# Optimization experiments

Measured on AMD Instinct MI355X. Metric: run time of the kernel, lower is better.

## Reference

```python
import jax, jax.numpy as jnp
import numpy as np

Z, K, HID = 128, 256, 512  # z_size, key_size, hidden_size


def setup_inputs() -> dict:
    key = jax.random.key(0)
    ks = jax.random.split(key, 12)
    B, T, Hi, Wi, Y = 512, 32, 32, 32, 4
    D = Hi * Wi
    s = 0.02
    f32 = jnp.float32
    return {
        "x_seq": jax.random.normal(ks[0], (B, T, Hi, Wi), f32),
        "W_enc": jax.random.normal(ks[1], (D, Z), f32) * s,
        "b_enc": jnp.zeros((Z,), f32),
        "W_lstm": jax.random.normal(ks[2], (K + 1, 4 * HID), f32) * s,
        "U_lstm": jax.random.normal(ks[3], (HID, 4 * HID), f32) * s,
        "b_lstm": jnp.zeros((4 * HID,), f32),
        "W_key": jax.random.normal(ks[4], (HID, K), f32) * s,
        "b_key": jnp.zeros((K,), f32),
        "W_g": jax.random.normal(ks[5], (HID, 1), f32) * s,
        "b_g": jnp.zeros((1,), f32),
        "W_y": jax.random.normal(ks[6], (HID, Y), f32) * s,
        "b_y": jnp.zeros((Y,), f32),
        "gamma": jnp.ones((Z,), f32),
        "beta": jnp.zeros((Z,), f32),
        "conf_gain": jnp.float32(1.0),
        "conf_bias": jnp.float32(0.0),
    }


def _forward(x_seq, W_enc, b_enc, W_lstm, U_lstm, b_lstm, W_key, b_key,
             W_g, b_g, W_y, b_y, gamma, beta, conf_gain, conf_bias):
    B, T = x_seq.shape[0], x_seq.shape[1]
    N = T + 1  # memory slots after final null step
    x = x_seq.reshape(B, T, -1)
    z = jax.nn.relu(x @ W_enc + b_enc)  # (B,T,Z) encoder stand-in
    # Faithful to TF source: list of (B,Z) stacks to (T,B,Z) and reduce axis 1
    # -> normalization is over the BATCH axis.
    mu = jnp.mean(z, axis=0, keepdims=True)
    var = jnp.var(z, axis=0, keepdims=True)
    z = (z - mu) / jnp.sqrt(var + 1e-8) * gamma + beta
    z_full = jnp.concatenate([z, jnp.zeros((B, 1, Z), z.dtype)], axis=1)  # (B,N,Z)

    def lstm_cell(x_in, h_in, c_in):
        gates = x_in @ W_lstm + h_in @ U_lstm + b_lstm
        i, f, g_, o = jnp.split(gates, 4, axis=-1)  # keras gate order i,f,c,o
        c_new = jax.nn.sigmoid(f) * c_in + jax.nn.sigmoid(i) * jnp.tanh(g_)
        h_new = jax.nn.sigmoid(o) * jnp.tanh(c_new)
        return h_new, c_new

    slot_ids = jnp.arange(N)

    def step(carry, inp):
        h, c, key_r, M_k, M_v = carry
        z_t, t = inp  # z_t: (B,Z), t: scalar step index
        # Faithful: source passes initial_state=(cell_state, hidden), swapping roles.
        h_new, c_new = lstm_cell(key_r, c, h)
        key_w = jax.nn.relu(h_new @ W_key + b_key)          # (B,K)
        g = jax.nn.sigmoid(h_new @ W_g + b_g)               # (B,1)
        y_lin = jax.nn.softmax(h_new @ W_y + b_y, axis=-1)  # (B,Y)
        # content-addressable read over the t filled slots
        sim = jnp.einsum('bz,bnz->bn', z_t, M_v)            # (B,N)
        mask = (slot_ids < t)[None, :]
        w_k = jax.nn.softmax(jnp.where(mask, sim, -1e9), axis=1)
        c_k = jax.nn.sigmoid(sim * conf_gain + conf_bias)   # (B,N)
        mem = jnp.concatenate([M_k, c_k[..., None]], axis=2)  # (B,N,K+1)
        weighted = jnp.einsum('bn,bnp->bp', w_k, mem)       # (B,K+1)
        key_r_new = jnp.where(t == 0, jnp.zeros_like(key_r), g * weighted)
        # write into slot t (pre-allocated memory, masked read above)
        M_k = M_k.at[:, t, :].set(key_w)
        M_v = M_v.at[:, t, :].set(z_t)
        return (h_new, c_new, key_r_new, M_k, M_v), y_lin

    h0 = jnp.zeros((B, HID), z.dtype)
    c0 = jnp.zeros((B, HID), z.dtype)
    kr0 = jnp.zeros((B, K + 1), z.dtype)
    Mk0 = jnp.zeros((B, N, K), z.dtype)
    Mv0 = jnp.zeros((B, N, Z), z.dtype)
    xs = (jnp.swapaxes(z_full, 0, 1), slot_ids)
    _, ys = jax.lax.scan(step, (h0, c0, kr0, Mk0, Mv0), xs)
    return ys[-1]  # y_pred_linear from the final (null-input) step


def reference(x_seq, W_enc, b_enc, W_lstm, U_lstm, b_lstm, W_key, b_key,
              W_g, b_g, W_y, b_y, gamma, beta, conf_gain, conf_bias):
    return _forward(x_seq, W_enc, b_enc, W_lstm, U_lstm, b_lstm, W_key, b_key,
                    W_g, b_g, W_y, b_y, gamma, beta, conf_gain, conf_bias)
```

## Files before the change

kernel.cpp:

```cpp
#include <hip/hip_runtime.h>

typedef __attribute__((ext_vector_type(8))) short short8;
typedef __attribute__((ext_vector_type(4))) float f32x4;
typedef __attribute__((ext_vector_type(8))) unsigned short ushort8;
typedef __attribute__((ext_vector_type(4))) unsigned short ushort4v;

__device__ __forceinline__ unsigned short f2bf(float f) {
  union { float f; unsigned u; } v; v.f = f;
  unsigned u = v.u;
  u += 0x7fffu + ((u >> 16) & 1u);
  return (unsigned short)(u >> 16);
}
__device__ __forceinline__ float sigm(float x) { return 1.f / (1.f + __expf(-x)); }
__device__ __forceinline__ float ftanh(float x) { return 1.f - 2.f / (__expf(2.f * x) + 1.f); }

__device__ __forceinline__ void gl16(const unsigned short* g, unsigned short* l) {
  __builtin_amdgcn_global_load_lds((const __attribute__((address_space(1))) void*)g,
                                   (__attribute__((address_space(3))) void*)l, 16, 0, 0);
}

__device__ __forceinline__ uint4 ld16_sys(const void* base, int off) {
  uint4 r;
  asm volatile("global_load_dwordx4 %0, %1, %2 sc0 sc1"
               : "=v"(r) : "v"(off), "s"(base) : "memory");
  return r;
}
__device__ __forceinline__ uint4 ld16_asm(const void* base, int off) {
  uint4 r;
  asm volatile("global_load_dwordx4 %0, %1, %2"
               : "=v"(r) : "v"(off), "s"(base) : "memory");
  return r;
}
__device__ __forceinline__ float ldf_sys(const void* base, int off) {
  float r;
  asm volatile("global_load_dword %0, %1, %2 sc0 sc1"
               : "=v"(r) : "v"(off), "s"(base) : "memory");
  return r;
}
__device__ __forceinline__ unsigned ldu_sys(const void* base, int off) {
  unsigned r;
  asm volatile("global_load_dword %0, %1, %2 sc0 sc1"
               : "=v"(r) : "v"(off), "s"(base) : "memory");
  return r;
}
__device__ __forceinline__ void stf_sys(void* base, int off, float v) {
  asm volatile("global_store_dword %0, %1, %2 sc0 sc1"
               :: "v"(off), "v"(v), "s"(base) : "memory");
}
__device__ __forceinline__ void stu_sys(void* base, int off, unsigned v) {
  asm volatile("global_store_dword %0, %1, %2 sc0 sc1"
               :: "v"(off), "v"(v), "s"(base) : "memory");
}
__device__ __forceinline__ void sth_sys(void* base, int off, unsigned short v) {
  asm volatile("global_store_short %0, %1, %2 sc0 sc1"
               :: "v"(off), "v"(v), "s"(base) : "memory");
}
#define WAITVM(N)                                          \
  asm volatile("s_waitcnt vmcnt(" #N ")" ::: "memory");    \
  __builtin_amdgcn_sched_barrier(0)

__device__ __forceinline__ void gbar(unsigned* flags, unsigned gen) {
  asm volatile("s_waitcnt vmcnt(0)" ::: "memory");
  __syncthreads();
  if (threadIdx.x == 0) stu_sys(flags, (int)(blockIdx.x * 64), gen);
  int off = (int)(threadIdx.x * 64);
  for (;;) {
    unsigned v = ldu_sys(flags, off);
    asm volatile("s_waitcnt vmcnt(0)" ::: "memory");
    if (v >= gen) break;
    __builtin_amdgcn_s_sleep(1);
  }
  __syncthreads();
}

#define LSTR 40

__global__ void k_prep(const float* __restrict__ W_lstm, const float* __restrict__ U_lstm,
                       const float* __restrict__ W_enc, const float* __restrict__ W_key,
                       const float* __restrict__ W_g, const float* __restrict__ W_y,
                       const float* __restrict__ b_key, const float* __restrict__ b_g,
                       const float* __restrict__ b_y,
                       unsigned short* __restrict__ WcombT, unsigned short* __restrict__ Wk2T,
                       unsigned short* __restrict__ WencT, float* __restrict__ bias2,
                       unsigned short* __restrict__ xinA, unsigned short* __restrict__ xinB,
                       float* __restrict__ h, float* __restrict__ z_full,
                       unsigned* __restrict__ bar) {
  const int N1 = 2048 * 800, N2 = 320 * 512, N3 = 128 * 1024, N4 = 320,
            N5 = 512 * 800, N7 = 512 * 512, N8 = 512 * 128, N9 = 4096;
  int i = blockIdx.x * 256 + threadIdx.x;
  if (i < N1) {
    int np = i / 800, k = i - np * 800;
    int j = np >> 2, gate = np & 3, n = gate * 512 + j;
    float v = 0.f;
    if (k < 257) v = W_lstm[k * 2048 + n];
    else if (k >= 288) v = U_lstm[(k - 288) * 2048 + n];
    WcombT[i] = f2bf(v);
    return;
  }
  i -= N1;
  if (i < N2) {
    int n = i / 512, k = i - n * 512;
    float v = 0.f;
    if (n < 256) v = W_key[k * 256 + n];
    else if (n == 256) v = W_g[k];
    else if (n < 261) v = W_y[k * 4 + (n - 257)];
    Wk2T[i] = f2bf(v);
    return;
  }
  i -= N2;
  if (i < N3) {
    int n = i / 1024, k = i - n * 1024;
    WencT[i] = f2bf(W_enc[k * 128 + n]);
    return;
  }
  i -= N3;
  if (i < N4) {
    float v = (i < 256) ? b_key[i] : (i == 256 ? b_g[0] : (i < 261 ? b_y[i - 257] : 0.f));
    bias2[i] = v;
    return;
  }
  i -= N4;
  if (i < N5) { xinA[i] = 0; return; }
  i -= N5;
  if (i < N5) { xinB[i] = 0; return; }
  i -= N5;
  if (i < N7) { h[i] = 0.f; return; }
  i -= N7;
  if (i < N8) {
    int b = i >> 7, z = i & 127;
    z_full[(b * 33 + 32) * 128 + z] = 0.f;
    return;
  }
  i -= N8;
  if (i < N9) bar[i] = 0;
}

__global__ __launch_bounds__(512) void k_enc(const float* __restrict__ x,
                                             const unsigned short* __restrict__ WencT,
                                             const float* __restrict__ b_enc,
                                             float* __restrict__ zbuf) {
  __shared__ __align__(16) unsigned short As[2][64 * LSTR];
  __shared__ __align__(16) unsigned short Bs[2][128 * LSTR];
  int tid = threadIdx.x;
  int m0 = blockIdx.x * 64;
  int lane = tid & 63, wid = tid >> 6;
  int wm = (wid >> 2) * 32, wn = (wid & 3) * 32;
  int q = lane >> 4, r = lane & 15;
  int ldrowA = tid >> 3, ldcA = (tid & 7) * 4;
  int ldrowB = tid >> 2, ldcB = (tid & 3) * 8;
  const float4* Ag = reinterpret_cast<const float4*>(x + (size_t)(m0 + ldrowA) * 1024);
  const uint4* Bg = reinterpret_cast<const uint4*>(WencT + (size_t)ldrowB * 1024);
  float4 ra = Ag[ldcA >> 2];
  uint4 rb = Bg[ldcB >> 3];
  f32x4 acc[2][2] = {};
  int s = 0;
  {
    ushort4v t4;
    t4[0] = f2bf(ra.x); t4[1] = f2bf(ra.y); t4[2] = f2bf(ra.z); t4[3] = f2bf(ra.w);
    *reinterpret_cast<ushort4v*>(&As[0][ldrowA * LSTR + ldcA]) = t4;
    *reinterpret_cast<uint4*>(&Bs[0][ldrowB * LSTR + ldcB]) = rb;
  }
  __syncthreads();
  for (int kk = 0; kk < 32; ++kk) {
    if (kk < 31) {
      int k0 = (kk + 1) * 32;
      ra = Ag[(k0 + ldcA) >> 2];
      rb = Bg[(k0 + ldcB) >> 3];
    }
    short8 a0 = *reinterpret_cast<const short8*>(&As[s][(wm + r) * LSTR + q * 8]);
    short8 a1 = *reinterpret_cast<const short8*>(&As[s][(wm + 16 + r) * LSTR + q * 8]);
    short8 b0 = *reinterpret_cast<const short8*>(&Bs[s][(wn + r) * LSTR + q * 8]);
    short8 b1 = *reinterpret_cast<const short8*>(&Bs[s][(wn + 16 + r) * LSTR + q * 8]);
    acc[0][0] = __builtin_amdgcn_mfma_f32_16x16x32_bf16(a0, b0, acc[0][0], 0, 0, 0);
    acc[0][1] = __builtin_amdgcn_mfma_f32_16x16x32_bf16(a0, b1, acc[0][1], 0, 0, 0);
    acc[1][0] = __builtin_amdgcn_mfma_f32_16x16x32_bf16(a1, b0, acc[1][0], 0, 0, 0);
    acc[1][1] = __builtin_amdgcn_mfma_f32_16x16x32_bf16(a1, b1, acc[1][1], 0, 0, 0);
    if (kk < 31) {
      ushort4v t4;
      t4[0] = f2bf(ra.x); t4[1] = f2bf(ra.y); t4[2] = f2bf(ra.z); t4[3] = f2bf(ra.w);
      *reinterpret_cast<ushort4v*>(&As[s ^ 1][ldrowA * LSTR + ldcA]) = t4;
      *reinterpret_cast<uint4*>(&Bs[s ^ 1][ldrowB * LSTR + ldcB]) = rb;
      s ^= 1;
    }
    __syncthreads();
  }
#pragma unroll
  for (int mt = 0; mt < 2; ++mt)
#pragma unroll
    for (int nt = 0; nt < 2; ++nt)
#pragma unroll
      for (int e = 0; e < 4; ++e) {
        int row = m0 + wm + mt * 16 + q * 4 + e;
        int col = wn + nt * 16 + r;
        zbuf[(size_t)row * 128 + col] = fmaxf(acc[mt][nt][e] + b_enc[col], 0.f);
      }
}

__global__ __launch_bounds__(256) void k_ln(const float* __restrict__ zbuf,
                                            const float* __restrict__ gamma,
                                            const float* __restrict__ beta,
                                            float* __restrict__ z_full) {
  int bid = blockIdx.x;
  int tstep = bid >> 3;
  int z0 = (bid & 7) * 16;
  int tid = threadIdx.x;
  int zl = tid & 15, bg = tid >> 4;
  __shared__ float ps[256], qs[256];
  __shared__ float muS[16], rsS[16];
  float s = 0.f, ss = 0.f;
  for (int ii = 0; ii < 32; ++ii) {
    int b = bg * 32 + ii;
    float v = zbuf[(size_t)(b * 32 + tstep) * 128 + z0 + zl];
    s += v; ss += v * v;
  }
  ps[tid] = s; qs[tid] = ss;
  __syncthreads();
  if (tid < 16) {
    float S = 0.f, Q = 0.f;
    for (int g2 = 0; g2 < 16; ++g2) { S += ps[g2 * 16 + tid]; Q += qs[g2 * 16 + tid]; }
    float mu = S / 512.f;
    float var = Q / 512.f - mu * mu;
    muS[tid] = mu;
    rsS[tid] = rsqrtf(var + 1e-8f);
  }
  __syncthreads();
  float ga = gamma[z0 + zl], be = beta[z0 + zl];
  float mu = muS[zl], rs = rsS[zl];
  for (int ii = 0; ii < 32; ++ii) {
    int b = bg * 32 + ii;
    float v = zbuf[(size_t)(b * 32 + tstep) * 128 + z0 + zl];
    z_full[(size_t)(b * 33 + tstep) * 128 + z0 + zl] = (v - mu) * rs * ga + be;
  }
}

__global__ __launch_bounds__(256) void k_attnpre(const float* __restrict__ z_full,
                                                 const float* __restrict__ cgain,
                                                 const float* __restrict__ cbias,
                                                 float* __restrict__ wk_tbl,
                                                 float* __restrict__ wck_tbl) {
  __shared__ float zs[33 * 128];
  __shared__ float sim[33 * 33];
  int b = blockIdx.x, tid = threadIdx.x;
  const float* zb = z_full + (size_t)b * 33 * 128;
  for (int i = tid; i < 33 * 128; i += 256) zs[i] = zb[i];
  __syncthreads();
  for (int p = tid; p < 33 * 33; p += 256) {
    int t = p / 33, n = p - t * 33;
    float s = 0.f;
    if (n < t) {
#pragma unroll 8
      for (int k2 = 0; k2 < 128; ++k2) s += zs[t * 128 + k2] * zs[n * 128 + k2];
    }
    sim[p] = s;
  }
  __syncthreads();
  if (tid >= 1 && tid < 33) {
    int t = tid;
    float cg = cgain[0], cb2 = cbias[0];
    float m = -3.0e38f;
    for (int n = 0; n < t; ++n) m = fmaxf(m, sim[t * 33 + n]);
    float ssum = 0.f;
    for (int n = 0; n < t; ++n) ssum += __expf(sim[t * 33 + n] - m);
    float inv = 1.f / ssum;
    float wck = 0.f;
    for (int n = 0; n < t; ++n) {
      float wk = __expf(sim[t * 33 + n] - m) * inv;
      wk_tbl[((size_t)b * 33 + t) * 33 + n] = wk;
      float ck = 1.f / (1.f + __expf(-(sim[t * 33 + n] * cg + cb2)));
      wck += wk * ck;
    }
    wck_tbl[b * 33 + t] = wck;
  }
}

__global__ __launch_bounds__(256) void k_loop(
    unsigned short* __restrict__ xinA, unsigned short* __restrict__ xinB,
    const unsigned short* __restrict__ WT, const float* __restrict__ b_lstm,
    float* __restrict__ h, unsigned short* __restrict__ hbf,
    const unsigned short* __restrict__ Wk2T, const float* __restrict__ bias2,
    float* __restrict__ Mk, float* __restrict__ logits,
    const float* __restrict__ Wg, const float* __restrict__ bg,
    const float* __restrict__ wk_tbl, const float* __restrict__ wck_tbl,
    float* __restrict__ out, unsigned* __restrict__ bar) {
  __shared__ __align__(16) unsigned short Bres[64 * 808];
  __shared__ __align__(16) unsigned char scr[43136];
  const int tid = threadIdx.x, bid = blockIdx.x;
  const int lane = tid & 63, w = tid >> 6;
  const int q = lane >> 4, r = lane & 15;
  const int wm = (w >> 1) * 32, wn = (w & 1) * 32;
  const int nn = bid & 31, mi = bid >> 5;
  const int m0 = mi * 64, n0g = nn * 64;
  unsigned gen = 0;

  for (int l = 0; l < 26; ++l) {
    int gw = l * 256 + w * 64;
    if (gw < 6464) {
      int g = gw + lane;
      int row = g / 101, cg = g - row * 101;
      int col = (cg >= 100) ? 792 : cg * 8;
      gl16(WT + (size_t)(n0g + row) * 800 + col, Bres + gw * 8);
    }
  }

  int srow[5], scol[5];
#pragma unroll
  for (int l = 0; l < 5; ++l) {
    int idx = l * 256 + tid;
    srow[l] = idx / 20;
    scol[l] = (idx - srow[l] * 20) * 8;
  }
  unsigned short* A0 = (unsigned short*)scr;
  unsigned short* A1 = (unsigned short*)(scr + 21504);

  const int jl = tid & 15, jg = nn * 16 + jl, rl0 = tid >> 4;
  const float bL0 = b_lstm[jg], bL1 = b_lstm[512 + jg],
              bL2 = b_lstm[1024 + jg], bL3 = b_lstm[1536 + jg];
  float hreg[4] = {0.f, 0.f, 0.f, 0.f};

  const int mi2 = bid / 5, ni2 = bid - mi2 * 5;

  asm volatile("s_waitcnt vmcnt(0)" ::: "memory");
  __syncthreads();

  for (int t = 0; t < 33; ++t) {
    const unsigned short* cur = (t & 1) ? xinB : xinA;
    unsigned short* nxt = (t & 1) ? xinA : xinB;

    uint4 R[5];
#pragma unroll
    for (int l = 0; l < 5; ++l)
      R[l] = ld16_sys(cur, ((m0 + srow[l]) * 800 + scol[l]) * 2);
    asm volatile("s_waitcnt vmcnt(0)" ::: "memory");
    __builtin_amdgcn_sched_barrier(0);
#pragma unroll
    for (int l = 0; l < 5; ++l)
      *(uint4*)&A0[srow[l] * 168 + scol[l]] = R[l];
    __syncthreads();

    f32x4 acc[2][2] = {};
    for (int c = 0; c < 5; ++c) {
      const unsigned short* Ac = (c & 1) ? A1 : A0;
      unsigned short* An = (c & 1) ? A0 : A1;
      if (c < 4) {
#pragma unroll
        for (int l = 0; l < 5; ++l)
          R[l] = ld16_sys(cur, ((m0 + srow[l]) * 800 + (c + 1) * 160 + scol[l]) * 2);
      }
#pragma unroll
      for (int ks = 0; ks < 5; ++ks) {
        short8 a0 = *(const short8*)&Ac[(wm + r) * 168 + ks * 32 + q * 8];
        short8 a1 = *(const short8*)&Ac[(wm + 16 + r) * 168 + ks * 32 + q * 8];
        short8 b0 = *(const short8*)&Bres[(wn + r) * 808 + c * 160 + ks * 32 + q * 8];
        short8 b1 = *(const short8*)&Bres[(wn + 16 + r) * 808 + c * 160 + ks * 32 + q * 8];
        acc[0][0] = __builtin_amdgcn_mfma_f32_16x16x32_bf16(a0, b0, acc[0][0], 0, 0, 0);
        acc[0][1] = __builtin_amdgcn_mfma_f32_16x16x32_bf16(a0, b1, acc[0][1], 0, 0, 0);
        acc[1][0] = __builtin_amdgcn_mfma_f32_16x16x32_bf16(a1, b0, acc[1][0], 0, 0, 0);
        acc[1][1] = __builtin_amdgcn_mfma_f32_16x16x32_bf16(a1, b1, acc[1][1], 0, 0, 0);
      }
      if (c < 4) {
        asm volatile("s_waitcnt vmcnt(0)" ::: "memory");
        __builtin_amdgcn_sched_barrier(0);
#pragma unroll
        for (int l = 0; l < 5; ++l)
          *(uint4*)&An[srow[l] * 168 + scol[l]] = R[l];
        __syncthreads();
      }
    }
    __syncthreads();

    float* Cs = (float*)scr;
#pragma unroll
    for (int mt = 0; mt < 2; ++mt)
#pragma unroll
      for (int nt = 0; nt < 2; ++nt)
#pragma unroll
        for (int e = 0; e < 4; ++e)
          Cs[(wm + mt * 16 + q * 4 + e) * 65 + wn + nt * 16 + r] = acc[mt][nt][e];
    __syncthreads();
#pragma unroll
    for (int it = 0; it < 4; ++it) {
      int rl = it * 16 + rl0;
      int brow = m0 + rl;
      float gi = Cs[rl * 65 + jl * 4 + 0] + bL0;
      float gf = Cs[rl * 65 + jl * 4 + 1] + bL1;
      float gc = Cs[rl * 65 + jl * 4 + 2] + bL2;
      float go = Cs[rl * 65 + jl * 4 + 3] + bL3;
      float cnew = sigm(gf) * hreg[it] + sigm(gi) * ftanh(gc);
      float hnew = sigm(go) * ftanh(cnew);
      hreg[it] = hnew;
      stf_sys(h, (brow * 512 + jg) * 4, hnew);
      sth_sys(hbf, (brow * 512 + jg) * 2, f2bf(hnew));
      sth_sys(nxt, (brow * 800 + 288 + jg) * 2, f2bf(cnew));
    }
    ++gen; gbar(bar, gen);

    if (bid < 40) {
      int m0b = mi2 * 64, n0b = ni2 * 64;
      int aoff0 = ((m0b + wm + r) * 512 + q * 8) * 2;
      int aoff1 = aoff0 + 16 * 1024;
      int boff0 = ((n0b + wn + r) * 512 + q * 8) * 2;
      int boff1 = boff0 + 16 * 1024;
      uint4 ab[4][2], bb[4][2];
      f32x4 acc2[2][2] = {};
#pragma unroll
      for (int j = 0; j < 3; ++j) {
        ab[j][0] = ld16_sys(hbf, aoff0 + j * 64);
        ab[j][1] = ld16_sys(hbf, aoff1 + j * 64);
        bb[j][0] = ld16_asm(Wk2T, boff0 + j * 64);
        bb[j][1] = ld16_asm(Wk2T, boff1 + j * 64);
      }
#pragma unroll
      for (int kk = 0; kk < 16; ++kk) {
        if (kk < 13) {
          int j = kk + 3;
          ab[j & 3][0] = ld16_sys(hbf, aoff0 + j * 64);
          ab[j & 3][1] = ld16_sys(hbf, aoff1 + j * 64);
          bb[j & 3][0] = ld16_asm(Wk2T, boff0 + j * 64);
          bb[j & 3][1] = ld16_asm(Wk2T, boff1 + j * 64);
        }
        if (kk < 13) { WAITVM(12); }
        else if (kk == 13) { WAITVM(8); }
        else if (kk == 14) { WAITVM(4); }
        else { WAITVM(0); }
        short8 a0 = *(const short8*)&ab[kk & 3][0];
        short8 a1 = *(const short8*)&ab[kk & 3][1];
        short8 b0s = *(const short8*)&bb[kk & 3][0];
        short8 b1s = *(const short8*)&bb[kk & 3][1];
        acc2[0][0] = __builtin_amdgcn_mfma_f32_16x16x32_bf16(a0, b0s, acc2[0][0], 0, 0, 0);
        acc2[0][1] = __builtin_amdgcn_mfma_f32_16x16x32_bf16(a0, b1s, acc2[0][1], 0, 0, 0);
        acc2[1][0] = __builtin_amdgcn_mfma_f32_16x16x32_bf16(a1, b0s, acc2[1][0], 0, 0, 0);
        acc2[1][1] = __builtin_amdgcn_mfma_f32_16x16x32_bf16(a1, b1s, acc2[1][1], 0, 0, 0);
      }
#pragma unroll
      for (int mt = 0; mt < 2; ++mt)
#pragma unroll
        for (int nt = 0; nt < 2; ++nt)
#pragma unroll
          for (int e2 = 0; e2 < 4; ++e2) {
            int row = m0b + wm + mt * 16 + q * 4 + e2;
            int np = n0b + wn + nt * 16 + r;
            float v = acc2[mt][nt][e2] + bias2[np];
            if (np < 256)
              stf_sys(Mk, ((row * 33 + t) * 256 + np) * 4, fmaxf(v, 0.f));
            else if (np >= 257 && np < 261)
              stf_sys(logits, (row * 4 + (np - 257)) * 4, v);
          }
    } else if (t > 0 && t < 32) {
      float* wkS = (float*)scr;
      float* red4 = (float*)(scr + 512);
      for (int rr = 0; rr < 3; ++rr) {
        int b = (bid - 40) + 216 * rr;
        if (b < 512) {
          float ha = ldf_sys(h, (b * 512 + tid) * 4);
          float hb = ldf_sys(h, (b * 512 + 256 + tid) * 4);
          asm volatile("s_waitcnt vmcnt(0)" ::: "memory");
          float sd = ha * Wg[tid] + hb * Wg[256 + tid];
#pragma unroll
          for (int off = 32; off > 0; off >>= 1) sd += __shfl_down(sd, off);
          if (lane == 0) red4[w] = sd;
          if (tid < t) wkS[tid] = wk_tbl[((size_t)b * 33 + t) * 33 + tid];
          __syncthreads();
          float g = 1.f / (1.f + __expf(-(red4[0] + red4[1] + red4[2] + red4[3] + bg[0])));
          float p0 = 0.f, p1 = 0.f, p2 = 0.f, p3 = 0.f;
          int n = 0;
          for (; n + 4 <= t; n += 4) {
            p0 += wkS[n] * Mk[((size_t)b * 33 + n) * 256 + tid];
            p1 += wkS[n + 1] * Mk[((size_t)b * 33 + n + 1) * 256 + tid];
            p2 += wkS[n + 2] * Mk[((size_t)b * 33 + n + 2) * 256 + tid];
            p3 += wkS[n + 3] * Mk[((size_t)b * 33 + n + 3) * 256 + tid];
          }
          for (; n < t; ++n) p0 += wkS[n] * Mk[((size_t)b * 33 + n) * 256 + tid];
          sth_sys(nxt, (b * 800 + tid) * 2, f2bf(g * ((p0 + p1) + (p2 + p3))));
          if (tid == 0) sth_sys(nxt, (b * 800 + 256) * 2, f2bf(g * wck_tbl[b * 33 + t]));
          __syncthreads();
        }
      }
    }
    ++gen; gbar(bar, gen);
  }
  if (bid == 0) {
    for (int r2 = tid; r2 < 512; r2 += 256) {
      float a = ldf_sys(logits, r2 * 16);
      float b2 = ldf_sys(logits, r2 * 16 + 4);
      float c2 = ldf_sys(logits, r2 * 16 + 8);
      float d2 = ldf_sys(logits, r2 * 16 + 12);
      asm volatile("s_waitcnt vmcnt(0)" ::: "memory");
      float m = fmaxf(fmaxf(a, b2), fmaxf(c2, d2));
      float ea = __expf(a - m), eb = __expf(b2 - m), ec = __expf(c2 - m), ed = __expf(d2 - m);
      float ssum = ea + eb + ec + ed;
      out[r2 * 4] = ea / ssum; out[r2 * 4 + 1] = eb / ssum;
      out[r2 * 4 + 2] = ec / ssum; out[r2 * 4 + 3] = ed / ssum;
    }
  }
}

__global__ __launch_bounds__(256) void k_gates(const unsigned short* __restrict__ xin,
                                               const unsigned short* __restrict__ WT,
                                               const float* __restrict__ b_lstm,
                                               float* __restrict__ h,
                                               unsigned short* __restrict__ hbf,
                                               unsigned short* __restrict__ xin_nxt) {
  __shared__ __align__(16) unsigned short As[2][64 * LSTR];
  __shared__ __align__(16) unsigned short Bs[2][64 * LSTR];
  __shared__ float Cs[64 * 65];
  int tid = threadIdx.x;
  int nn = blockIdx.x;
  int m0 = blockIdx.y * 64;
  int n0 = nn * 64;
  int lane = tid & 63, wid = tid >> 6;
  int wm = (wid >> 1) * 32, wn = (wid & 1) * 32;
  int q = lane >> 4, r = lane & 15;
  int ldrow = tid >> 2, ldc = (tid & 3) * 8;
  const uint4* Ag = reinterpret_cast<const uint4*>(xin + (size_t)(m0 + ldrow) * 800);
  const uint4* Bg = reinterpret_cast<const uint4*>(WT + (size_t)(n0 + ldrow) * 800);
  uint4 ra = Ag[ldc >> 3], rb = Bg[ldc >> 3];
  f32x4 acc[2][2] = {};
  int s = 0;
  *reinterpret_cast<uint4*>(&As[0][ldrow * LSTR + ldc]) = ra;
  *reinterpret_cast<uint4*>(&Bs[0][ldrow * LSTR + ldc]) = rb;
  __syncthreads();
  for (int kk = 0; kk < 25; ++kk) {
    if (kk < 24) {
      int k0 = (kk + 1) * 32;
      ra = Ag[(k0 + ldc) >> 3];
      rb = Bg[(k0 + ldc) >> 3];
    }
    short8 a0 = *reinterpret_cast<const short8*>(&As[s][(wm + r) * LSTR + q * 8]);
    short8 a1 = *reinterpret_cast<const short8*>(&As[s][(wm + 16 + r) * LSTR + q * 8]);
    short8 b0 = *reinterpret_cast<const short8*>(&Bs[s][(wn + r) * LSTR + q * 8]);
    short8 b1 = *reinterpret_cast<const short8*>(&Bs[s][(wn + 16 + r) * LSTR + q * 8]);
    acc[0][0] = __builtin_amdgcn_mfma_f32_16x16x32_bf16(a0, b0, acc[0][0], 0, 0, 0);
    acc[0][1] = __builtin_amdgcn_mfma_f32_16x16x32_bf16(a0, b1, acc[0][1], 0, 0, 0);
    acc[1][0] = __builtin_amdgcn_mfma_f32_16x16x32_bf16(a1, b0, acc[1][0], 0, 0, 0);
    acc[1][1] = __builtin_amdgcn_mfma_f32_16x16x32_bf16(a1, b1, acc[1][1], 0, 0, 0);
    if (kk < 24) {
      *reinterpret_cast<uint4*>(&As[s ^ 1][ldrow * LSTR + ldc]) = ra;
      *reinterpret_cast<uint4*>(&Bs[s ^ 1][ldrow * LSTR + ldc]) = rb;
      s ^= 1;
    }
    __syncthreads();
  }
#pragma unroll
  for (int mt = 0; mt < 2; ++mt)
#pragma unroll
    for (int nt = 0; nt < 2; ++nt)
#pragma unroll
      for (int e = 0; e < 4; ++e)
        Cs[(wm + mt * 16 + q * 4 + e) * 65 + wn + nt * 16 + r] = acc[mt][nt][e];
  __syncthreads();
#pragma unroll
  for (int it = 0; it < 4; ++it) {
    int id = it * 256 + tid;
    int rl = id >> 4, jl = id & 15;
    int brow = m0 + rl;
    int j = nn * 16 + jl;
    float gi = Cs[rl * 65 + jl * 4 + 0] + b_lstm[j];
    float gf = Cs[rl * 65 + jl * 4 + 1] + b_lstm[512 + j];
    float gg = Cs[rl * 65 + jl * 4 + 2] + b_lstm[1024 + j];
    float go = Cs[rl * 65 + jl * 4 + 3] + b_lstm[1536 + j];
    float hold = h[brow * 512 + j];
    float cnew = sigm(gf) * hold + sigm(gi) * ftanh(gg);
    float hnew = sigm(go) * ftanh(cnew);
    h[brow * 512 + j] = hnew;
    hbf[brow * 512 + j] = f2bf(hnew);
    xin_nxt[brow * 800 + 288 + j] = f2bf(cnew);
  }
}

__global__ __launch_bounds__(256) void k_head(const unsigned short* __restrict__ hbf,
                                              const unsigned short* __restrict__ Wk2T,
                                              const float* __restrict__ bias2,
                                              float* __restrict__ Mk,
                                              float* __restrict__ logits,
                                              const float* __restrict__ h,
                                              const float* __restrict__ Wg,
                                              const float* __restrict__ bg,
                                              const float* __restrict__ wk_tbl,
                                              const float* __restrict__ wck_tbl,
                                              unsigned short* __restrict__ xin_nxt,
                                              int t) {
  __shared__ __align__(16) unsigned short As[2][64 * LSTR];
  __shared__ __align__(16) unsigned short Bs[2][64 * LSTR];
  __shared__ float wkS[33];
  __shared__ float red[256];
  int bid = blockIdx.x;
  int tid = threadIdx.x;
  if (bid < 40) {
    int mi = bid / 5, ni = bid - mi * 5;
    int m0 = mi * 64, n0 = ni * 64;
    int lane = tid & 63, wid = tid >> 6;
    int wm = (wid >> 1) * 32, wn = (wid & 1) * 32;
    int q = lane >> 4, r = lane & 15;
    int ldrow = tid >> 2, ldc = (tid & 3) * 8;
    const uint4* Ag = reinterpret_cast<const uint4*>(hbf + (size_t)(m0 + ldrow) * 512);
    const uint4* Bg = reinterpret_cast<const uint4*>(Wk2T + (size_t)(n0 + ldrow) * 512);
    uint4 ra = Ag[ldc >> 3], rb = Bg[ldc >> 3];
    f32x4 acc[2][2] = {};
    int s = 0;
    *reinterpret_cast<uint4*>(&As[0][ldrow * LSTR + ldc]) = ra;
    *reinterpret_cast<uint4*>(&Bs[0][ldrow * LSTR + ldc]) = rb;
    __syncthreads();
    for (int kk = 0; kk < 16; ++kk) {
      if (kk < 15) {
        int k0 = (kk + 1) * 32;
        ra = Ag[(k0 + ldc) >> 3];
        rb = Bg[(k0 + ldc) >> 3];
      }
      short8 a0 = *reinterpret_cast<const short8*>(&As[s][(wm + r) * LSTR + q * 8]);
      short8 a1 = *reinterpret_cast<const short8*>(&As[s][(wm + 16 + r) * LSTR + q * 8]);
      short8 b0 = *reinterpret_cast<const short8*>(&Bs[s][(wn + r) * LSTR + q * 8]);
      short8 b1 = *reinterpret_cast<const short8*>(&Bs[s][(wn + 16 + r) * LSTR + q * 8]);
      acc[0][0] = __builtin_amdgcn_mfma_f32_16x16x32_bf16(a0, b0, acc[0][0], 0, 0, 0);
      acc[0][1] = __builtin_amdgcn_mfma_f32_16x16x32_bf16(a0, b1, acc[0][1], 0, 0, 0);
      acc[1][0] = __builtin_amdgcn_mfma_f32_16x16x32_bf16(a1, b0, acc[1][0], 0, 0, 0);
      acc[1][1] = __builtin_amdgcn_mfma_f32_16x16x32_bf16(a1, b1, acc[1][1], 0, 0, 0);
      if (kk < 15) {
        *reinterpret_cast<uint4*>(&As[s ^ 1][ldrow * LSTR + ldc]) = ra;
        *reinterpret_cast<uint4*>(&Bs[s ^ 1][ldrow * LSTR + ldc]) = rb;
        s ^= 1;
      }
      __syncthreads();
    }
#pragma unroll
    for (int mt = 0; mt < 2; ++mt)
#pragma unroll
      for (int nt = 0; nt < 2; ++nt)
#pragma unroll
        for (int e = 0; e < 4; ++e) {
          int row = m0 + wm + mt * 16 + q * 4 + e;
          int np = n0 + wn + nt * 16 + r;
          float v = acc[mt][nt][e] + bias2[np];
          if (np < 256) Mk[(size_t)(row * 33 + t) * 256 + np] = fmaxf(v, 0.f);
          else if (np >= 257 && np < 261) logits[row * 4 + (np - 257)] = v;
        }
  } else {
    if (t == 0 || t == 32) return;
    int b = bid - 40;
    float s = h[b * 512 + tid] * Wg[tid] + h[b * 512 + 256 + tid] * Wg[256 + tid];
    red[tid] = s;
    if (tid < t) wkS[tid] = wk_tbl[((size_t)b * 33 + t) * 33 + tid];
    __syncthreads();
    for (int off = 128; off > 0; off >>= 1) {
      if (tid < off) red[tid] += red[tid + off];
      __syncthreads();
    }
    float g = 1.f / (1.f + __expf(-(red[0] + bg[0])));
    float acc = 0.f;
    for (int n = 0; n < t; ++n) acc += wkS[n] * Mk[((size_t)b * 33 + n) * 256 + tid];
    xin_nxt[b * 800 + tid] = f2bf(g * acc);
    if (tid == 0) xin_nxt[b * 800 + 256] = f2bf(g * wck_tbl[b * 33 + t]);
  }
}

__global__ void k_softmax(const float* __restrict__ logits, float* __restrict__ out) {
  int tid = threadIdx.x;
  for (int r2 = tid; r2 < 512; r2 += 256) {
    float a = logits[r2 * 4], b = logits[r2 * 4 + 1], c = logits[r2 * 4 + 2], d = logits[r2 * 4 + 3];
    float m = fmaxf(fmaxf(a, b), fmaxf(c, d));
    float ea = __expf(a - m), eb = __expf(b - m), ec = __expf(c - m), ed = __expf(d - m);
    float s = ea + eb + ec + ed;
    out[r2 * 4] = ea / s; out[r2 * 4 + 1] = eb / s;
    out[r2 * 4 + 2] = ec / s; out[r2 * 4 + 3] = ed / s;
  }
}

extern "C" void kernel_launch(void* const* d_in, const int* in_sizes, int n_in,
                              void* d_out, int out_size, void* d_ws, size_t ws_size,
                              hipStream_t stream) {
  const float* x_seq = (const float*)d_in[0];
  const float* W_enc = (const float*)d_in[1];
  const float* b_enc = (const float*)d_in[2];
  const float* W_lstm = (const float*)d_in[3];
  const float* U_lstm = (const float*)d_in[4];
  const float* b_lstm = (const float*)d_in[5];
  const float* W_key = (const float*)d_in[6];
  const float* b_key = (const float*)d_in[7];
  const float* W_g = (const float*)d_in[8];
  const float* b_g = (const float*)d_in[9];
  const float* W_y = (const float*)d_in[10];
  const float* b_y = (const float*)d_in[11];
  const float* gamma = (const float*)d_in[12];
  const float* beta = (const float*)d_in[13];
  const float* cg_ = (const float*)d_in[14];
  const float* cb = (const float*)d_in[15];

  char* p = (char*)d_ws;
  auto alloc = [&](size_t bytes) {
    char* r = p;
    p += (bytes + 255) & ~(size_t)255;
    return r;
  };
  float* zbuf = (float*)alloc((size_t)16384 * 128 * 4);
  float* z_full = (float*)alloc((size_t)512 * 33 * 128 * 4);
  unsigned short* WcombT = (unsigned short*)alloc((size_t)2048 * 800 * 2);
  unsigned short* WencT = (unsigned short*)alloc((size_t)128 * 1024 * 2);
  unsigned short* Wk2T = (unsigned short*)alloc((size_t)320 * 512 * 2);
  float* bias2 = (float*)alloc(320 * 4);
  unsigned short* xinA = (unsigned short*)alloc((size_t)512 * 800 * 2);
  unsigned short* xinB = (unsigned short*)alloc((size_t)512 * 800 * 2);
  float* h = (float*)alloc((size_t)512 * 512 * 4);
  unsigned short* hbf = (unsigned short*)alloc((size_t)512 * 512 * 2);
  float* Mk = (float*)alloc((size_t)512 * 33 * 256 * 4);
  float* logits = (float*)alloc((size_t)512 * 4 * 4);
  float* wk_tbl = (float*)alloc((size_t)512 * 33 * 33 * 4);
  float* wck_tbl = (float*)alloc((size_t)512 * 33 * 4);
  unsigned* bar = (unsigned*)alloc(16384);
  float* outp = (float*)d_out;

  const int prep_total = 2048 * 800 + 320 * 512 + 128 * 1024 + 320 + 2 * 512 * 800 +
                         512 * 512 + 512 * 128 + 4096;
  k_prep<<<(prep_total + 255) / 256, 256, 0, stream>>>(
      W_lstm, U_lstm, W_enc, W_key, W_g, W_y, b_key, b_g, b_y,
      WcombT, Wk2T, WencT, bias2, xinA, xinB, h, z_full, bar);
  k_enc<<<256, 512, 0, stream>>>(x_seq, WencT, b_enc, zbuf);
  k_ln<<<256, 256, 0, stream>>>(zbuf, gamma, beta, z_full);
  k_attnpre<<<512, 256, 0, stream>>>(z_full, cg_, cb, wk_tbl, wck_tbl);

  void* cargs[16];
  cargs[0] = &xinA;  cargs[1] = &xinB;   cargs[2] = &WcombT; cargs[3] = &b_lstm;
  cargs[4] = &h;     cargs[5] = &hbf;    cargs[6] = &Wk2T;   cargs[7] = &bias2;
  cargs[8] = &Mk;    cargs[9] = &logits; cargs[10] = &W_g;   cargs[11] = &b_g;
  cargs[12] = &wk_tbl; cargs[13] = &wck_tbl; cargs[14] = &outp; cargs[15] = &bar;
  hipError_t ce = hipLaunchCooperativeKernel((const void*)k_loop, dim3(256), dim3(256),
                                             cargs, 0u, stream);
  if (ce != hipSuccess) {
    for (int t = 0; t < 33; ++t) {
      unsigned short* cur = (t & 1) ? xinB : xinA;
      unsigned short* nxt = (t & 1) ? xinA : xinB;
      k_gates<<<dim3(32, 8), 256, 0, stream>>>(cur, WcombT, b_lstm, h, hbf, nxt);
      k_head<<<552, 256, 0, stream>>>(hbf, Wk2T, bias2, Mk, logits, h,
                                      W_g, b_g, wk_tbl, wck_tbl, nxt, t);
    }
    k_softmax<<<1, 256, 0, stream>>>(logits, outp);
  }
}
```

Measured before the change: 782.7 us.

## Replace grid-wide barrier with per-batch-group barriers and fuse final softmax

Each group of 32 blocks owning the same 64 batch rows now does the gate GEMM, key projection and attention read for those rows, so the barrier only waits on the group's 32 flags instead of all 256 blocks. The key head now skips the logits column tile except on the final step, and that last step computes the softmax directly instead of a separate single-block pass after the loop. The trailing barrier on the last step is dropped. This cuts cross-CU synchronisation cost and per-step work, at the cost of a less even split of the attention work across blocks.

```diff
diff --git a/kernel.cpp b/kernel.cpp
--- a/kernel.cpp
+++ b/kernel.cpp
@@ -59,11 +59,12 @@
   asm volatile("s_waitcnt vmcnt(" #N ")" ::: "memory");    \
   __builtin_amdgcn_sched_barrier(0)
 
-__device__ __forceinline__ void gbar(unsigned* flags, unsigned gen) {
+__device__ __forceinline__ void gbar_grp(unsigned* flags, unsigned gen,
+                                         int myslot, int pollslot) {
   asm volatile("s_waitcnt vmcnt(0)" ::: "memory");
   __syncthreads();
-  if (threadIdx.x == 0) stu_sys(flags, (int)(blockIdx.x * 64), gen);
-  int off = (int)(threadIdx.x * 64);
+  if (threadIdx.x == 0) stu_sys(flags, myslot * 64, gen);
+  int off = pollslot * 64;
   for (;;) {
     unsigned v = ldu_sys(flags, off);
     asm volatile("s_waitcnt vmcnt(0)" ::: "memory");
@@ -278,25 +279,26 @@
     const unsigned short* __restrict__ WT, const float* __restrict__ b_lstm,
     float* __restrict__ h, unsigned short* __restrict__ hbf,
     const unsigned short* __restrict__ Wk2T, const float* __restrict__ bias2,
-    float* __restrict__ Mk, float* __restrict__ logits,
-    const float* __restrict__ Wg, const float* __restrict__ bg,
-    const float* __restrict__ wk_tbl, const float* __restrict__ wck_tbl,
-    float* __restrict__ out, unsigned* __restrict__ bar) {
+    float* __restrict__ Mk, const float* __restrict__ Wg,
+    const float* __restrict__ bg, const float* __restrict__ wk_tbl,
+    const float* __restrict__ wck_tbl, float* __restrict__ out,
+    unsigned* __restrict__ bar) {
   __shared__ __align__(16) unsigned short Bres[64 * 808];
   __shared__ __align__(16) unsigned char scr[43136];
   const int tid = threadIdx.x, bid = blockIdx.x;
   const int lane = tid & 63, w = tid >> 6;
   const int q = lane >> 4, r = lane & 15;
   const int wm = (w >> 1) * 32, wn = (w & 1) * 32;
-  const int nn = bid & 31, mi = bid >> 5;
-  const int m0 = mi * 64, n0g = nn * 64;
+  const int nn = bid & 31, g = bid >> 5;
+  const int m0 = g * 64, n0g = nn * 64;
+  const int pollslot = (g << 5) + (tid & 31);
   unsigned gen = 0;
 
   for (int l = 0; l < 26; ++l) {
     int gw = l * 256 + w * 64;
     if (gw < 6464) {
-      int g = gw + lane;
-      int row = g / 101, cg = g - row * 101;
+      int gg = gw + lane;
+      int row = gg / 101, cg = gg - row * 101;
       int col = (cg >= 100) ? 792 : cg * 8;
       gl16(WT + (size_t)(n0g + row) * 800 + col, Bres + gw * 8);
     }
@@ -316,8 +318,6 @@
   const float bL0 = b_lstm[jg], bL1 = b_lstm[512 + jg],
               bL2 = b_lstm[1024 + jg], bL3 = b_lstm[1536 + jg];
   float hreg[4] = {0.f, 0.f, 0.f, 0.f};
-
-  const int mi2 = bid / 5, ni2 = bid - mi2 * 5;
 
   asm volatile("s_waitcnt vmcnt(0)" ::: "memory");
   __syncthreads();
@@ -392,65 +392,94 @@
       sth_sys(hbf, (brow * 512 + jg) * 2, f2bf(hnew));
       sth_sys(nxt, (brow * 800 + 288 + jg) * 2, f2bf(cnew));
     }
-    ++gen; gbar(bar, gen);
-
-    if (bid < 40) {
-      int m0b = mi2 * 64, n0b = ni2 * 64;
-      int aoff0 = ((m0b + wm + r) * 512 + q * 8) * 2;
-      int aoff1 = aoff0 + 16 * 1024;
-      int boff0 = ((n0b + wn + r) * 512 + q * 8) * 2;
-      int boff1 = boff0 + 16 * 1024;
-      uint4 ab[4][2], bb[4][2];
-      f32x4 acc2[2][2] = {};
-#pragma unroll
-      for (int j = 0; j < 3; ++j) {
-        ab[j][0] = ld16_sys(hbf, aoff0 + j * 64);
-        ab[j][1] = ld16_sys(hbf, aoff1 + j * 64);
-        bb[j][0] = ld16_asm(Wk2T, boff0 + j * 64);
-        bb[j][1] = ld16_asm(Wk2T, boff1 + j * 64);
+    ++gen; gbar_grp(bar, gen, bid, pollslot);
+
+    if (nn < 5) {
+      if (nn < 4 || t == 32) {
+        int m0b = g * 64, n0b = nn * 64;
+        int aoff0 = ((m0b + wm + r) * 512 + q * 8) * 2;
+        int aoff1 = aoff0 + 16 * 1024;
+        int boff0 = ((n0b + wn + r) * 512 + q * 8) * 2;
+        int boff1 = boff0 + 16 * 1024;
+        uint4 ab[4][2], bb[4][2];
+        f32x4 acc2[2][2] = {};
+#pragma unroll
+        for (int j = 0; j < 3; ++j) {
+          ab[j][0] = ld16_sys(hbf, aoff0 + j * 64);
+          ab[j][1] = ld16_sys(hbf, aoff1 + j * 64);
+          bb[j][0] = ld16_asm(Wk2T, boff0 + j * 64);
+          bb[j][1] = ld16_asm(Wk2T, boff1 + j * 64);
+        }
+#pragma unroll
+        for (int kk = 0; kk < 16; ++kk) {
+          if (kk < 13) {
+            int j = kk + 3;
+            ab[j & 3][0] = ld16_sys(hbf, aoff0 + j * 64);
+            ab[j & 3][1] = ld16_sys(hbf, aoff1 + j * 64);
+            bb[j & 3][0] = ld16_asm(Wk2T, boff0 + j * 64);
+            bb[j & 3][1] = ld16_asm(Wk2T, boff1 + j * 64);
+          }
+          if (kk < 13) { WAITVM(12); }
+          else if (kk == 13) { WAITVM(8); }
+          else if (kk == 14) { WAITVM(4); }
+          else { WAITVM(0); }
+          short8 a0 = *(const short8*)&ab[kk & 3][0];
+          short8 a1 = *(const short8*)&ab[kk & 3][1];
+          short8 b0s = *(const short8*)&bb[kk & 3][0];
+          short8 b1s = *(const short8*)&bb[kk & 3][1];
+          acc2[0][0] = __builtin_amdgcn_mfma_f32_16x16x32_bf16(a0, b0s, acc2[0][0], 0, 0, 0);
+          acc2[0][1] = __builtin_amdgcn_mfma_f32_16x16x32_bf16(a0, b1s, acc2[0][1], 0, 0, 0);
+          acc2[1][0] = __builtin_amdgcn_mfma_f32_16x16x32_bf16(a1, b0s, acc2[1][0], 0, 0, 0);
+          acc2[1][1] = __builtin_amdgcn_mfma_f32_16x16x32_bf16(a1, b1s, acc2[1][1], 0, 0, 0);
+        }
+        if (nn < 4) {
+          if (t < 32) {
+#pragma unroll
+            for (int mt = 0; mt < 2; ++mt)
+#pragma unroll
+              for (int nt = 0; nt < 2; ++nt)
+#pragma unroll
+                for (int e2 = 0; e2 < 4; ++e2) {
+                  int row = m0b + wm + mt * 16 + q * 4 + e2;
+                  int np = n0b + wn + nt * 16 + r;
+                  stf_sys(Mk, ((row * 33 + t) * 256 + np) * 4,
+                          fmaxf(acc2[mt][nt][e2] + bias2[np], 0.f));
+                }
+          }
+        } else {
+          float* ylds = (float*)scr;
+#pragma unroll
+          for (int mt = 0; mt < 2; ++mt)
+#pragma unroll
+            for (int nt = 0; nt < 2; ++nt)
+#pragma unroll
+              for (int e2 = 0; e2 < 4; ++e2) {
+                int rowl = wm + mt * 16 + q * 4 + e2;
+                int np = n0b + wn + nt * 16 + r;
+                if (np >= 257 && np < 261)
+                  ylds[rowl * 4 + (np - 257)] = acc2[mt][nt][e2] + bias2[np];
+              }
+          __syncthreads();
+          if (tid < 64) {
+            float a = ylds[tid * 4], b2 = ylds[tid * 4 + 1],
+                  c2 = ylds[tid * 4 + 2], d2 = ylds[tid * 4 + 3];
+            float m = fmaxf(fmaxf(a, b2), fmaxf(c2, d2));
+            float ea = __expf(a - m), eb = __expf(b2 - m),
+                  ec = __expf(c2 - m), ed = __expf(d2 - m);
+            float inv = 1.f / (ea + eb + ec + ed);
+            int row = m0b + tid;
+            out[row * 4] = ea * inv; out[row * 4 + 1] = eb * inv;
+            out[row * 4 + 2] = ec * inv; out[row * 4 + 3] = ed * inv;
+          }
+        }
       }
-#pragma unroll
-      for (int kk = 0; kk < 16; ++kk) {
-        if (kk < 13) {
-          int j = kk + 3;
-          ab[j & 3][0] = ld16_sys(hbf, aoff0 + j * 64);
-          ab[j & 3][1] = ld16_sys(hbf, aoff1 + j * 64);
-          bb[j & 3][0] = ld16_asm(Wk2T, boff0 + j * 64);
-          bb[j & 3][1] = ld16_asm(Wk2T, boff1 + j * 64);
-        }
-        if (kk < 13) { WAITVM(12); }
-        else if (kk == 13) { WAITVM(8); }
-        else if (kk == 14) { WAITVM(4); }
-        else { WAITVM(0); }
-        short8 a0 = *(const short8*)&ab[kk & 3][0];
-        short8 a1 = *(const short8*)&ab[kk & 3][1];
-        short8 b0s = *(const short8*)&bb[kk & 3][0];
-        short8 b1s = *(const short8*)&bb[kk & 3][1];
-        acc2[0][0] = __builtin_amdgcn_mfma_f32_16x16x32_bf16(a0, b0s, acc2[0][0], 0, 0, 0);
-        acc2[0][1] = __builtin_amdgcn_mfma_f32_16x16x32_bf16(a0, b1s, acc2[0][1], 0, 0, 0);
-        acc2[1][0] = __builtin_amdgcn_mfma_f32_16x16x32_bf16(a1, b0s, acc2[1][0], 0, 0, 0);
-        acc2[1][1] = __builtin_amdgcn_mfma_f32_16x16x32_bf16(a1, b1s, acc2[1][1], 0, 0, 0);
-      }
-#pragma unroll
-      for (int mt = 0; mt < 2; ++mt)
-#pragma unroll
-        for (int nt = 0; nt < 2; ++nt)
-#pragma unroll
-          for (int e2 = 0; e2 < 4; ++e2) {
-            int row = m0b + wm + mt * 16 + q * 4 + e2;
-            int np = n0b + wn + nt * 16 + r;
-            float v = acc2[mt][nt][e2] + bias2[np];
-            if (np < 256)
-              stf_sys(Mk, ((row * 33 + t) * 256 + np) * 4, fmaxf(v, 0.f));
-            else if (np >= 257 && np < 261)
-              stf_sys(logits, (row * 4 + (np - 257)) * 4, v);
-          }
     } else if (t > 0 && t < 32) {
       float* wkS = (float*)scr;
       float* red4 = (float*)(scr + 512);
       for (int rr = 0; rr < 3; ++rr) {
-        int b = (bid - 40) + 216 * rr;
-        if (b < 512) {
+        int idx = (nn - 5) + 27 * rr;
+        if (idx < 64) {
+          int b = m0 + idx;
           float ha = ldf_sys(h, (b * 512 + tid) * 4);
           float hb = ldf_sys(h, (b * 512 + 256 + tid) * 4);
           asm volatile("s_waitcnt vmcnt(0)" ::: "memory");
@@ -460,7 +489,7 @@
           if (lane == 0) red4[w] = sd;
           if (tid < t) wkS[tid] = wk_tbl[((size_t)b * 33 + t) * 33 + tid];
           __syncthreads();
-          float g = 1.f / (1.f + __expf(-(red4[0] + red4[1] + red4[2] + red4[3] + bg[0])));
+          float gv = 1.f / (1.f + __expf(-(red4[0] + red4[1] + red4[2] + red4[3] + bg[0])));
           float p0 = 0.f, p1 = 0.f, p2 = 0.f, p3 = 0.f;
           int n = 0;
           for (; n + 4 <= t; n += 4) {
@@ -470,27 +499,13 @@
             p3 += wkS[n + 3] * Mk[((size_t)b * 33 + n + 3) * 256 + tid];
           }
           for (; n < t; ++n) p0 += wkS[n] * Mk[((size_t)b * 33 + n) * 256 + tid];
-          sth_sys(nxt, (b * 800 + tid) * 2, f2bf(g * ((p0 + p1) + (p2 + p3))));
-          if (tid == 0) sth_sys(nxt, (b * 800 + 256) * 2, f2bf(g * wck_tbl[b * 33 + t]));
+          sth_sys(nxt, (b * 800 + tid) * 2, f2bf(gv * ((p0 + p1) + (p2 + p3))));
+          if (tid == 0) sth_sys(nxt, (b * 800 + 256) * 2, f2bf(gv * wck_tbl[b * 33 + t]));
           __syncthreads();
         }
       }
     }
-    ++gen; gbar(bar, gen);
-  }
-  if (bid == 0) {
-    for (int r2 = tid; r2 < 512; r2 += 256) {
-      float a = ldf_sys(logits, r2 * 16);
-      float b2 = ldf_sys(logits, r2 * 16 + 4);
-      float c2 = ldf_sys(logits, r2 * 16 + 8);
-      float d2 = ldf_sys(logits, r2 * 16 + 12);
-      asm volatile("s_waitcnt vmcnt(0)" ::: "memory");
-      float m = fmaxf(fmaxf(a, b2), fmaxf(c2, d2));
-      float ea = __expf(a - m), eb = __expf(b2 - m), ec = __expf(c2 - m), ed = __expf(d2 - m);
-      float ssum = ea + eb + ec + ed;
-      out[r2 * 4] = ea / ssum; out[r2 * 4 + 1] = eb / ssum;
-      out[r2 * 4 + 2] = ec / ssum; out[r2 * 4 + 3] = ed / ssum;
-    }
+    if (t < 32) { ++gen; gbar_grp(bar, gen, bid, pollslot); }
   }
 }
 
@@ -716,11 +731,11 @@
   k_ln<<<256, 256, 0, stream>>>(zbuf, gamma, beta, z_full);
   k_attnpre<<<512, 256, 0, stream>>>(z_full, cg_, cb, wk_tbl, wck_tbl);
 
-  void* cargs[16];
+  void* cargs[15];
   cargs[0] = &xinA;  cargs[1] = &xinB;   cargs[2] = &WcombT; cargs[3] = &b_lstm;
   cargs[4] = &h;     cargs[5] = &hbf;    cargs[6] = &Wk2T;   cargs[7] = &bias2;
-  cargs[8] = &Mk;    cargs[9] = &logits; cargs[10] = &W_g;   cargs[11] = &b_g;
-  cargs[12] = &wk_tbl; cargs[13] = &wck_tbl; cargs[14] = &outp; cargs[15] = &bar;
+  cargs[8] = &Mk;    cargs[9] = &W_g;    cargs[10] = &b_g;   cargs[11] = &wk_tbl;
+  cargs[12] = &wck_tbl; cargs[13] = &outp; cargs[14] = &bar;
   hipError_t ce = hipLaunchCooperativeKernel((const void*)k_loop, dim3(256), dim3(256),
                                              cargs, 0u, stream);
   if (ce != hipSuccess) {
```

Result: faster. 738.8 us (-5.6%).
